# Performance work log

Hardware: AMD Instinct MI355X
Metric: run time of the kernel (lower is better)

Reference implementation:

```python
import jax, jax.numpy as jnp
import numpy as np

EPS = 1e-12  # matches torch F.normalize default eps


def _idx(k, pad, stride, size):
    o = (size + 2 * pad - k) // stride + 1
    return (jnp.arange(o) * stride)[:, None] + jnp.arange(k)[None, :], o  # [o, k]


def unfold(x, k, pad, stride):
    # x: [B, C, H, W] -> [B, C*k*k, oh*ow], torch F.unfold ordering (c slowest, then kh, kw)
    B, C, H, W = x.shape
    xp = jnp.pad(x, ((0, 0), (0, 0), (pad, pad), (pad, pad)))
    ri, oh = _idx(k, pad, stride, H)
    ci, ow = _idx(k, pad, stride, W)
    p = xp[:, :, ri[:, None, :, None], ci[None, :, None, :]]  # [B, C, oh, ow, k, k]
    return p.transpose(0, 1, 4, 5, 2, 3).reshape(B, C * k * k, oh * ow)


def fold(cols, out_hw, k, pad, stride):
    # inverse of unfold with overlap-add (torch F.fold)
    B, CKK, L = cols.shape
    C = CKK // (k * k)
    H, W = out_hw
    ri, oh = _idx(k, pad, stride, H)
    ci, ow = _idx(k, pad, stride, W)
    p = cols.reshape(B, C, k, k, oh, ow).transpose(0, 1, 4, 5, 2, 3)  # [B,C,oh,ow,k,k]
    canvas = jnp.zeros((B, C, H + 2 * pad, W + 2 * pad), cols.dtype)
    canvas = canvas.at[:, :, ri[:, None, :, None], ci[None, :, None, :]].add(p)
    return canvas[:, :, pad:pad + H, pad:pad + W]


def _l2norm(x, axis):
    n = jnp.sqrt(jnp.sum(x * x, axis=axis, keepdims=True))
    return x / jnp.maximum(n, EPS)


def setup_inputs() -> dict:
    key = jax.random.key(0)
    ks = jax.random.split(key, 5)
    return {
        "lrsr_lv3": jax.random.normal(ks[0], (1, 256, 48, 48), jnp.float32),
        "refsr_lv3": jax.random.normal(ks[1], (1, 256, 48, 48), jnp.float32),
        "ref_lv1": jax.random.normal(ks[2], (1, 64, 192, 192), jnp.float32),
        "ref_lv2": jax.random.normal(ks[3], (1, 128, 96, 96), jnp.float32),
        "ref_lv3": jax.random.normal(ks[4], (1, 256, 48, 48), jnp.float32),
    }


def reference(lrsr_lv3, refsr_lv3, ref_lv1, ref_lv2, ref_lv3):
    B, C, H, W = lrsr_lv3.shape
    lr_u = unfold(lrsr_lv3, 3, 1, 1)              # [B, C*9, L_lr]
    rf_u = unfold(refsr_lv3, 3, 1, 1)             # [B, C*9, L_ref]
    rf_n = _l2norm(rf_u.transpose(0, 2, 1), 2)    # [B, L_ref, C*9]
    lr_n = _l2norm(lr_u, 1)                       # [B, C*9, L_lr]
    R = jnp.einsum('brc,bcl->brl', rf_n, lr_n)    # [B, L_ref, L_lr] cosine corr
    R_star = jnp.max(R, axis=1)                   # [B, L_lr]
    R_arg = jnp.argmax(R, axis=1)                 # [B, L_lr]

    ref3_u = unfold(ref_lv3, 3, 1, 1)             # [B, C*9,   L_ref]
    ref2_u = unfold(ref_lv2, 6, 2, 2)             # [B, C2*36, L_ref]
    ref1_u = unfold(ref_lv1, 12, 4, 4)            # [B, C1*144,L_ref]

    idx = R_arg[:, None, :]                       # [B, 1, L_lr]
    T3_u = jnp.take_along_axis(ref3_u, idx, axis=2)
    T2_u = jnp.take_along_axis(ref2_u, idx, axis=2)
    T1_u = jnp.take_along_axis(ref1_u, idx, axis=2)

    T_lv3 = fold(T3_u, (H, W), 3, 1, 1) / 9.0
    T_lv2 = fold(T2_u, (H * 2, W * 2), 6, 2, 2) / 9.0
    T_lv1 = fold(T1_u, (H * 4, W * 4), 12, 4, 4) / 9.0
    S = R_star.reshape(B, 1, H, W)
    return (S, T_lv3, T_lv2, T_lv1)
```

## Files before the change

kernel.cpp:

```cpp
#include <hip/hip_runtime.h>
#include <hip/hip_bf16.h>
#include <math.h>

#define HW 48
#define NPOS 2304
#define CCH 256
#define PCOLS 2500
#define PLANESZ (NPOS * CCH)
#define KC 16
#define TM 128
#define TN 64

typedef __attribute__((ext_vector_type(8))) short short8v;
typedef __attribute__((ext_vector_type(16))) float f32x16;

__device__ inline void ph_ss2(int vb, const float* __restrict__ lr,
                              const float* __restrict__ ref, float* __restrict__ SS2,
                              float (*red)[64]) {
    const int img = vb / 36, bx = vb % 36;
    const float* imgp = img ? ref : lr;
    const int t = threadIdx.x;
    const int px = t & 63, cg = t >> 6;
    const int p = bx * 64 + px;
    const float* base = imgp + (size_t)cg * 64 * NPOS + p;
    float s = 0.f;
#pragma unroll 4
    for (int cc = 0; cc < 64; ++cc) {
        float v = base[(size_t)cc * NPOS];
        s = fmaf(v, v, s);
    }
    red[cg][px] = s;
    __syncthreads();
    if (cg == 0)
        SS2[img * NPOS + p] = red[0][px] + red[1][px] + red[2][px] + red[3][px];
}

__device__ inline void ph_split(int local, const float* __restrict__ lr,
                                const float* __restrict__ ref, ushort* __restrict__ planes) {
    const int img = local / 288;
    const int gid = (local % 288) * 256 + threadIdx.x;
    const float* src = img ? ref : lr;
    const int lane = gid & 63;
    const int k16  = (gid >> 6) & 15;
    const int blk  = gid >> 10;
    const int pos  = blk * 32 + (lane & 31);
    const int c0   = k16 * 16 + (lane >> 5) * 8;
    ushort h8[8], m8[8], l8[8];
#pragma unroll
    for (int e = 0; e < 8; ++e) {
        float a = src[(size_t)(c0 + e) * NPOS + pos];
        __hip_bfloat16 hb = __float2bfloat16(a);
        float hf = __bfloat162float(hb);
        float r1 = a - hf;
        __hip_bfloat16 mb = __float2bfloat16(r1);
        float mf = __bfloat162float(mb);
        __hip_bfloat16 lb = __float2bfloat16(r1 - mf);
        h8[e] = *(ushort*)&hb;
        m8[e] = *(ushort*)&mb;
        l8[e] = *(ushort*)&lb;
    }
    ushort* ph = planes + (size_t)(img * 3 + 0) * PLANESZ + (size_t)gid * 8;
    ushort* pm = planes + (size_t)(img * 3 + 1) * PLANESZ + (size_t)gid * 8;
    ushort* pl = planes + (size_t)(img * 3 + 2) * PLANESZ + (size_t)gid * 8;
#pragma unroll
    for (int e = 0; e < 8; ++e) { ph[e] = h8[e]; pm[e] = m8[e]; pl[e] = l8[e]; }
}

__device__ inline void ph_zero(int local, float* __restrict__ P) {
    const int idx = local * 256 + threadIdx.x;
    if (idx >= NPOS * 196) return;
    const int row = idx / 196, b = idx - row * 196;
    int pc;
    if (b < 50)       pc = b;
    else if (b < 100) pc = 2450 + (b - 50);
    else {
        const int i = b - 100;
        const int rr = 1 + (i >> 1);
        pc = rr * 50 + ((i & 1) ? 49 : 0);
    }
    P[(size_t)row * PCOLS + pc] = 0.f;
}

__global__ __launch_bounds__(256) void prep_kernel(const float* __restrict__ lr,
                                                   const float* __restrict__ ref,
                                                   float* __restrict__ SS2,
                                                   ushort* __restrict__ planes,
                                                   float* __restrict__ P,
                                                   int do_split) {
    __shared__ float red[4][64];
    const int b = blockIdx.x;
    if (do_split) {
        if (b < 72)        ph_ss2(b, lr, ref, SS2, red);
        else if (b < 648)  ph_split(b - 72, lr, ref, planes);
        else               ph_zero(b - 648, P);
    } else {
        if (b < 72)        ph_ss2(b, lr, ref, SS2, red);
        else               ph_zero(b - 72, P);
    }
}

__device__ inline void ph_invnorm(int vb, const float* __restrict__ SS2,
                                  float* __restrict__ inv2) {
    const int img = vb / 9;
    const int p = (vb % 9) * 256 + threadIdx.x;
    const float* SS = SS2 + img * NPOS;
    const int y = p / HW, x = p % HW;
    float s = 0.f;
#pragma unroll
    for (int di = -1; di <= 1; ++di) {
        int yy = y + di;
        if ((unsigned)yy >= HW) continue;
#pragma unroll
        for (int dj = -1; dj <= 1; ++dj) {
            int xx = x + dj;
            if ((unsigned)xx >= HW) continue;
            s += SS[yy * HW + xx];
        }
    }
    inv2[img * NPOS + p] = 1.f / fmaxf(sqrtf(s), 1e-12f);
}

__device__ inline void ph_gemm(int g, const ushort* __restrict__ planes,
                               float* __restrict__ P) {
    const int bxg = g % 36, byg = g / 36;
    const int t = threadIdx.x, lane = t & 63, w = t >> 6;
    const int nblk0 = bxg * 2;
    const int ablk  = byg * 4 + w;

    const ushort* baseA  = planes + ((size_t)(ablk * 16) * 64 + lane) * 8;
    const ushort* baseB0 = planes + (size_t)3 * PLANESZ + ((size_t)(nblk0 * 16) * 64 + lane) * 8;
    const ushort* baseB1 = baseB0 + 16 * 64 * 8;

    f32x16 acc0 = {};
    f32x16 acc1 = {};
#pragma unroll 4
    for (int k = 0; k < 16; ++k) {
        const int fo = k * 512;
        short8v ah = *(const short8v*)(baseA + fo);
        short8v am = *(const short8v*)(baseA + PLANESZ + fo);
        short8v al = *(const short8v*)(baseA + 2 * PLANESZ + fo);
        short8v bh0 = *(const short8v*)(baseB0 + fo);
        short8v bm0 = *(const short8v*)(baseB0 + PLANESZ + fo);
        short8v bl0 = *(const short8v*)(baseB0 + 2 * PLANESZ + fo);
        short8v bh1 = *(const short8v*)(baseB1 + fo);
        short8v bm1 = *(const short8v*)(baseB1 + PLANESZ + fo);
        short8v bl1 = *(const short8v*)(baseB1 + 2 * PLANESZ + fo);
        acc0 = __builtin_amdgcn_mfma_f32_32x32x16_bf16(ah, bh0, acc0, 0, 0, 0);
        acc0 = __builtin_amdgcn_mfma_f32_32x32x16_bf16(ah, bm0, acc0, 0, 0, 0);
        acc0 = __builtin_amdgcn_mfma_f32_32x32x16_bf16(am, bh0, acc0, 0, 0, 0);
        acc0 = __builtin_amdgcn_mfma_f32_32x32x16_bf16(ah, bl0, acc0, 0, 0, 0);
        acc0 = __builtin_amdgcn_mfma_f32_32x32x16_bf16(al, bh0, acc0, 0, 0, 0);
        acc0 = __builtin_amdgcn_mfma_f32_32x32x16_bf16(am, bm0, acc0, 0, 0, 0);
        acc1 = __builtin_amdgcn_mfma_f32_32x32x16_bf16(ah, bh1, acc1, 0, 0, 0);
        acc1 = __builtin_amdgcn_mfma_f32_32x32x16_bf16(ah, bm1, acc1, 0, 0, 0);
        acc1 = __builtin_amdgcn_mfma_f32_32x32x16_bf16(am, bh1, acc1, 0, 0, 0);
        acc1 = __builtin_amdgcn_mfma_f32_32x32x16_bf16(ah, bl1, acc1, 0, 0, 0);
        acc1 = __builtin_amdgcn_mfma_f32_32x32x16_bf16(al, bh1, acc1, 0, 0, 0);
        acc1 = __builtin_amdgcn_mfma_f32_32x32x16_bf16(am, bm1, acc1, 0, 0, 0);
    }
    const int m0 = byg * 128 + w * 32;
    const int half = lane >> 5;
    const int colA = nblk0 * 32 + (lane & 31);
    const int colB = colA + 32;
    const int pcA = (colA / 48) * 50 + colA % 48 + 51;
    const int pcB = (colB / 48) * 50 + colB % 48 + 51;
#pragma unroll
    for (int r = 0; r < 16; ++r) {
        const int row = (r & 3) + 8 * (r >> 2) + 4 * half;
        P[(size_t)(m0 + row) * PCOLS + pcA] = acc0[r];
        P[(size_t)(m0 + row) * PCOLS + pcB] = acc1[r];
    }
}

__global__ __launch_bounds__(256) void corr_kernel(const float* __restrict__ SS2,
                                                   float* __restrict__ inv2,
                                                   const ushort* __restrict__ planes,
                                                   float* __restrict__ P,
                                                   int do_gemm) {
    const int b = blockIdx.x;
    if (b < 18)          ph_invnorm(b, SS2, inv2);
    else if (do_gemm)    ph_gemm(b - 18, planes, P);
}

__global__ __launch_bounds__(256) void gemm_p_kernel(const float* __restrict__ lr,
                                                     const float* __restrict__ ref,
                                                     float* __restrict__ P) {
    __shared__ float As[KC][TM];
    __shared__ float Bs[KC][TN];
    const int t  = threadIdx.x;
    const int tx = t & 15, ty = t >> 4;
    const int lp0 = blockIdx.y * TM, rp0 = blockIdx.x * TN;
    const int ac0 = t >> 5,        acol0 = (t & 31) << 2;
    const int ac1 = (t + 256) >> 5, acol1 = acol0;
    const int bc = t >> 4, bcol = (t & 15) << 2;
    float acc[8][4] = {};
    for (int c0 = 0; c0 < CCH; c0 += KC) {
        float4 a0 = *(const float4*)(lr  + (size_t)(c0 + ac0) * NPOS + lp0 + acol0);
        float4 a1 = *(const float4*)(lr  + (size_t)(c0 + ac1) * NPOS + lp0 + acol1);
        float4 b0 = *(const float4*)(ref + (size_t)(c0 + bc)  * NPOS + rp0 + bcol);
        __syncthreads();
        *(float4*)&As[ac0][acol0] = a0;
        *(float4*)&As[ac1][acol1] = a1;
        *(float4*)&Bs[bc][bcol]   = b0;
        __syncthreads();
#pragma unroll
        for (int kk = 0; kk < KC; ++kk) {
            float4 aA = *(const float4*)&As[kk][ty * 8];
            float4 aB = *(const float4*)&As[kk][ty * 8 + 4];
            float4 bb = *(const float4*)&Bs[kk][tx * 4];
            const float av[8] = {aA.x, aA.y, aA.z, aA.w, aB.x, aB.y, aB.z, aB.w};
            const float bv[4] = {bb.x, bb.y, bb.z, bb.w};
#pragma unroll
            for (int i = 0; i < 8; ++i)
#pragma unroll
                for (int j = 0; j < 4; ++j)
                    acc[i][j] = fmaf(av[i], bv[j], acc[i][j]);
        }
    }
    const int col0 = rp0 + tx * 4;
    const int pc0  = (col0 / 48) * 50 + (col0 % 48) + 51;
#pragma unroll
    for (int i = 0; i < 8; ++i) {
        const int m = lp0 + ty * 8 + i;
        float4 v = make_float4(acc[i][0], acc[i][1], acc[i][2], acc[i][3]);
        __builtin_memcpy(P + (size_t)m * PCOLS + pc0, &v, 16);
    }
}

__global__ __launch_bounds__(192) void maxarg_kernel(const float* __restrict__ P,
                                                     const float* __restrict__ inr,
                                                     const float* __restrict__ inl,
                                                     float* __restrict__ S,
                                                     int* __restrict__ arg) {
    const int l  = blockIdx.x;
    const int yl = l / HW, xl = l % HW;
    const int t  = threadIdx.x;

    bool vmask[9];
    const float* bp[9];
#pragma unroll
    for (int d = 0; d < 9; ++d) {
        const int di = d / 3 - 1, dj = d % 3 - 1;
        vmask[d] = ((unsigned)(yl + di) < HW) && ((unsigned)(xl + dj) < HW);
        bp[d] = P + (ptrdiff_t)(l + di * HW + dj) * PCOLS + (di * 50 + dj);
    }

    float best = -1e30f;
    int bestr = 0;
#pragma unroll
    for (int vv = 0; vv < 3; ++vv) {
        const int v   = t + vv * 192;
        const int yr  = v / 12;
        const int xr4 = (v - yr * 12) << 2;
        const int q0  = yr * 50 + xr4 + 51;
        const int r0  = yr * HW + xr4;
        float4 a = make_float4(0.f, 0.f, 0.f, 0.f);
#pragma unroll
        for (int d = 0; d < 9; ++d) {
            if (vmask[d]) {
                float4 x;
                __builtin_memcpy(&x, bp[d] + q0, 16);
                a.x += x.x; a.y += x.y; a.z += x.z; a.w += x.w;
            }
        }
        const float4 w = *(const float4*)(inr + r0);
        const float vals[4] = {a.x * w.x, a.y * w.y, a.z * w.z, a.w * w.w};
#pragma unroll
        for (int k = 0; k < 4; ++k)
            if (vals[k] > best) { best = vals[k]; bestr = r0 + k; }
    }

    __shared__ float bv[256];
    __shared__ int   br[256];
    bv[t] = best; br[t] = bestr;
    if (t < 64) { bv[192 + t] = -1e30f; br[192 + t] = 0; }
    __syncthreads();
    for (int s2 = 128; s2 > 0; s2 >>= 1) {
        if (t < s2) {
            float v2 = bv[t + s2]; int r2 = br[t + s2];
            if (v2 > bv[t] || (v2 == bv[t] && r2 < br[t])) { bv[t] = v2; br[t] = r2; }
        }
        __syncthreads();
    }
    if (t == 0) {
        S[l]   = bv[0] * inl[l];
        arg[l] = br[0];
    }
}

template <int S_, int PAD, int H, int VEC, int CH>
__device__ inline void fold_vec(const float* __restrict__ ref, const int* __restrict__ arg,
                                float* __restrict__ out, int vecid, int cg) {
    const int x0 = (vecid * VEC) % H;
    const int y  = (vecid * VEC) / H;
    const int ty_ = (y + PAD) / S_;
    const int tx_ = (x0 + PAD) / S_;
    int off[9]; float w[9];
#pragma unroll
    for (int a = 0; a < 3; ++a) {
        const int oy = ty_ - a;
        const int di = y + PAD - S_ * oy;
#pragma unroll
    for (int b = 0; b < 3; ++b) {
            const int ox = tx_ - b;
            const int dj0 = x0 + PAD - S_ * ox;
            const int k = a * 3 + b;
            off[k] = 0; w[k] = 0.f;
            if ((unsigned)oy < HW && (unsigned)ox < HW) {
                const int ar = arg[oy * HW + ox];
                const int ry = ar / HW, rx = ar % HW;
                const int yy  = S_ * ry + di - PAD;
                const int xx0 = S_ * rx + dj0 - PAD;
                if ((unsigned)yy < H && (unsigned)xx0 < H) {
                    off[k] = yy * H + xx0;
                    w[k]   = 1.f / 9.f;
                }
            }
        }
    }
    const int c0 = cg * CH;
#pragma unroll
    for (int cc = 0; cc < CH; ++cc) {
        const float* bp = ref + (size_t)(c0 + cc) * (H * H);
        float acc[VEC] = {};
#pragma unroll
        for (int k = 0; k < 9; ++k) {
            float v[VEC];
            __builtin_memcpy(v, bp + off[k], VEC * 4);
#pragma unroll
            for (int i = 0; i < VEC; ++i) acc[i] = fmaf(w[k], v[i], acc[i]);
        }
        float* op = out + (size_t)(c0 + cc) * (H * H) + (size_t)y * H + x0;
        __builtin_memcpy(op, acc, VEC * 4);
    }
}

__global__ __launch_bounds__(256) void folds_kernel(const float* __restrict__ ref1,
                                                    const float* __restrict__ ref2,
                                                    const float* __restrict__ ref3,
                                                    const int* __restrict__ argb,
                                                    float* __restrict__ T1,
                                                    float* __restrict__ T2,
                                                    float* __restrict__ T3) {
    const int vb = blockIdx.x;
    if (vb < 576) {
        fold_vec<1, 1, 48, 1, 4>(ref3, argb, T3, (vb % 9) * 256 + threadIdx.x, vb / 9);
    } else if (vb < 1152) {
        const int lvb = vb - 576;
        fold_vec<2, 2, 96, 2, 4>(ref2, argb, T2, (lvb % 18) * 256 + threadIdx.x, lvb / 18);
    } else {
        const int lvb = vb - 1152;
        fold_vec<4, 4, 192, 4, 4>(ref1, argb, T1, (lvb % 36) * 256 + threadIdx.x, lvb / 36);
    }
}

extern "C" void kernel_launch(void* const* d_in, const int* in_sizes, int n_in,
                              void* d_out, int out_size, void* d_ws, size_t ws_size,
                              hipStream_t stream) {
    const float* lrsr  = (const float*)d_in[0];
    const float* refsr = (const float*)d_in[1];
    const float* ref1  = (const float*)d_in[2];
    const float* ref2  = (const float*)d_in[3];
    const float* ref3  = (const float*)d_in[4];

    float* out = (float*)d_out;
    float* S   = out;
    float* T3  = S  + NPOS;
    float* T2  = T3 + 256 * 48 * 48;
    float* T1  = T2 + 128 * 96 * 96;

    float*  P      = (float*)d_ws;
    float*  SS2    = P + (size_t)NPOS * PCOLS;
    float*  inv2   = SS2 + 2 * NPOS;
    int*    argb   = (int*)(inv2 + 2 * NPOS);
    ushort* planes = (ushort*)(argb + NPOS);
    float*  inl    = inv2;
    float*  inr    = inv2 + NPOS;

    const size_t need = ((size_t)NPOS * PCOLS + 5 * NPOS) * 4 + (size_t)6 * PLANESZ * 2;
    const int mfma_path = ws_size >= need ? 1 : 0;

    prep_kernel<<<mfma_path ? 2412 : 1836, 256, 0, stream>>>(lrsr, refsr, SS2, planes, P, mfma_path);

    if (mfma_path) {
        corr_kernel<<<666, 256, 0, stream>>>(SS2, inv2, planes, P, 1);
    } else {
        corr_kernel<<<18, 256, 0, stream>>>(SS2, inv2, planes, P, 0);
        gemm_p_kernel<<<dim3(NPOS / TN, NPOS / TM), 256, 0, stream>>>(lrsr, refsr, P);
    }

    maxarg_kernel<<<NPOS, 192, 0, stream>>>(P, inr, inl, S, argb);

    folds_kernel<<<1728, 256, 0, stream>>>(ref1, ref2, ref3, argb, T1, T2, T3);
}
```

Baseline: 94.02 us.

## Transpose reference features to pixel-major layout before gathering folds

Result: faster. 88.85 us (-5.5%).

```diff
diff --git a/kernel.cpp b/kernel.cpp
--- a/kernel.cpp
+++ b/kernel.cpp
@@ -288,70 +288,81 @@
     }
 }
 
-template <int S_, int PAD, int H, int VEC, int CH>
-__device__ inline void fold_vec(const float* __restrict__ ref, const int* __restrict__ arg,
-                                float* __restrict__ out, int vecid, int cg) {
-    const int x0 = (vecid * VEC) % H;
-    const int y  = (vecid * VEC) / H;
-    const int ty_ = (y + PAD) / S_;
-    const int tx_ = (x0 + PAD) / S_;
-    int off[9]; float w[9];
+__global__ __launch_bounds__(256) void transposeT_kernel(const float* __restrict__ ref1,
+                                                         const float* __restrict__ ref2,
+                                                         const float* __restrict__ ref3,
+                                                         float* __restrict__ T3t,
+                                                         float* __restrict__ T2t,
+                                                         float* __restrict__ T1t) {
+    __shared__ float tile[64][65];
+    const int b = blockIdx.x;
+    const float* src; float* dst; int C, NPIX, tpx, tch;
+    if (b < 144)      { src = ref3; dst = T3t; C = 256; NPIX = 2304;  tpx = b % 36;  tch = b / 36; }
+    else if (b < 432) { const int lb = b - 144; src = ref2; dst = T2t; C = 128; NPIX = 9216;  tpx = lb % 144; tch = lb / 144; }
+    else              { const int lb = b - 432; src = ref1; dst = T1t; C = 64;  NPIX = 36864; tpx = lb;       tch = 0; }
+    const int t = threadIdx.x;
+    const int px0 = tpx * 64, c0 = tch * 64;
+#pragma unroll
+    for (int r = 0; r < 16; ++r) {
+        const int cl = r * 4 + (t >> 6), pl = t & 63;
+        tile[cl][pl] = src[(size_t)(c0 + cl) * NPIX + px0 + pl];
+    }
+    __syncthreads();
+#pragma unroll
+    for (int r = 0; r < 16; ++r) {
+        const int pl = r * 4 + (t >> 6), cl = t & 63;
+        dst[(size_t)(px0 + pl) * C + c0 + cl] = tile[cl][pl];
+    }
+}
+
+template <int S_, int C, int H>
+__device__ inline void foldT(const float* __restrict__ refT, const int* __restrict__ arg,
+                             float* __restrict__ out, int u, int lane) {
+    const int y = u / 48, m = u % 48;
+    const int ty_ = y / S_ + 1;
+    float4 acc = make_float4(0.f, 0.f, 0.f, 0.f);
 #pragma unroll
     for (int a = 0; a < 3; ++a) {
         const int oy = ty_ - a;
-        const int di = y + PAD - S_ * oy;
-#pragma unroll
-    for (int b = 0; b < 3; ++b) {
-            const int ox = tx_ - b;
-            const int dj0 = x0 + PAD - S_ * ox;
-            const int k = a * 3 + b;
-            off[k] = 0; w[k] = 0.f;
-            if ((unsigned)oy < HW && (unsigned)ox < HW) {
-                const int ar = arg[oy * HW + ox];
-                const int ry = ar / HW, rx = ar % HW;
-                const int yy  = S_ * ry + di - PAD;
-                const int xx0 = S_ * rx + dj0 - PAD;
-                if ((unsigned)yy < H && (unsigned)xx0 < H) {
-                    off[k] = yy * H + xx0;
-                    w[k]   = 1.f / 9.f;
-                }
+        if ((unsigned)oy >= HW) continue;
+        const int di = y + S_ - S_ * oy;
+#pragma unroll
+        for (int b = 0; b < 3; ++b) {
+            const int ox = m + 1 - b;
+            if ((unsigned)ox >= HW) continue;
+            const int ar = arg[oy * HW + ox];
+            const int ry = ar / HW, rx = ar % HW;
+            const int yy  = S_ * ry + di - S_;
+            const int xx0 = S_ * (rx + b - 1);
+            if ((unsigned)yy < H && (unsigned)xx0 < H) {
+                float4 v;
+                __builtin_memcpy(&v, refT + ((size_t)yy * H + xx0) * C + lane * 4, 16);
+                acc.x += v.x; acc.y += v.y; acc.z += v.z; acc.w += v.w;
             }
         }
     }
-    const int c0 = cg * CH;
-#pragma unroll
-    for (int cc = 0; cc < CH; ++cc) {
-        const float* bp = ref + (size_t)(c0 + cc) * (H * H);
-        float acc[VEC] = {};
-#pragma unroll
-        for (int k = 0; k < 9; ++k) {
-            float v[VEC];
-            __builtin_memcpy(v, bp + off[k], VEC * 4);
-#pragma unroll
-            for (int i = 0; i < VEC; ++i) acc[i] = fmaf(w[k], v[i], acc[i]);
-        }
-        float* op = out + (size_t)(c0 + cc) * (H * H) + (size_t)y * H + x0;
-        __builtin_memcpy(op, acc, VEC * 4);
-    }
-}
-
-__global__ __launch_bounds__(256) void folds_kernel(const float* __restrict__ ref1,
-                                                    const float* __restrict__ ref2,
-                                                    const float* __restrict__ ref3,
+    const int idx = lane * 4;
+    const int xx = idx / C;
+    const int c  = idx % C;
+    const int x  = m * S_ + xx;
+    const float vals[4] = {acc.x, acc.y, acc.z, acc.w};
+    float* op = out + (size_t)c * (H * H) + (size_t)y * H + x;
+#pragma unroll
+    for (int e = 0; e < 4; ++e)
+        op[(size_t)e * (H * H)] = vals[e] * (1.f / 9.f);
+}
+
+__global__ __launch_bounds__(256) void foldT_kernel(const float* __restrict__ T1t,
+                                                    const float* __restrict__ T2t,
+                                                    const float* __restrict__ T3t,
                                                     const int* __restrict__ argb,
                                                     float* __restrict__ T1,
                                                     float* __restrict__ T2,
                                                     float* __restrict__ T3) {
-    const int vb = blockIdx.x;
-    if (vb < 576) {
-        fold_vec<1, 1, 48, 1, 4>(ref3, argb, T3, (vb % 9) * 256 + threadIdx.x, vb / 9);
-    } else if (vb < 1152) {
-        const int lvb = vb - 576;
-        fold_vec<2, 2, 96, 2, 4>(ref2, argb, T2, (lvb % 18) * 256 + threadIdx.x, lvb / 18);
-    } else {
-        const int lvb = vb - 1152;
-        fold_vec<4, 4, 192, 4, 4>(ref1, argb, T1, (lvb % 36) * 256 + threadIdx.x, lvb / 36);
-    }
+    const int b = blockIdx.x, w = threadIdx.x >> 6, lane = threadIdx.x & 63;
+    if (b < 576)        foldT<1, 256, 48>(T3t, argb, T3, b * 4 + w, lane);
+    else if (b < 1728)  foldT<2, 128, 96>(T2t, argb, T2, (b - 576) * 4 + w, lane);
+    else                foldT<4, 64, 192>(T1t, argb, T1, (b - 1728) * 4 + w, lane);
 }
 
 extern "C" void kernel_launch(void* const* d_in, const int* in_sizes, int n_in,
@@ -377,6 +388,10 @@
     float*  inl    = inv2;
     float*  inr    = inv2 + NPOS;
 
+    float* T3t = P;
+    float* T2t = T3t + 2304 * 256;
+    float* T1t = T2t + 9216 * 128;
+
     const size_t need = ((size_t)NPOS * PCOLS + 5 * NPOS) * 4 + (size_t)6 * PLANESZ * 2;
     const int mfma_path = ws_size >= need ? 1 : 0;
 
@@ -391,5 +406,7 @@
 
     maxarg_kernel<<<NPOS, 192, 0, stream>>>(P, inr, inl, S, argb);
 
-    folds_kernel<<<1728, 256, 0, stream>>>(ref1, ref2, ref3, argb, T1, T2, T3);
-}
+    transposeT_kernel<<<1008, 256, 0, stream>>>(ref1, ref2, ref3, T3t, T2t, T1t);
+
+    foldT_kernel<<<4032, 256, 0, stream>>>(T1t, T2t, T3t, argb, T1, T2, T3);
+}
```
